# Performance work log

Measured on AMD Instinct MI355X. Metric: run time of the kernel, lower is better.

## Reference

```python
import jax, jax.numpy as jnp
import numpy as np

T, H, W, C, HD, K = 4, 128, 128, 256, 8, 9
F = C // HD


def setup_inputs() -> dict:
    key = jax.random.key(0)
    ks = jax.random.split(key, 6)
    x = jax.random.normal(ks[0], (T, H, W, C), jnp.float32)
    attn = jax.random.uniform(ks[1], (1, HD, T, H, W, K), jnp.float32)
    attn = attn / attn.sum(-1, keepdims=True)  # softmax-normalized neighbor weights
    # integer flow offsets (dt, dh, dw) in [-3, 3], as produced by non-local search
    flows = jax.random.randint(ks[2], (1, HD, T, H, W, K, 3), -3, 4, jnp.int32)
    v_w = jax.random.normal(ks[3], (C, C), jnp.float32) * (C ** -0.5)
    proj_w = jax.random.normal(ks[4], (C, C), jnp.float32) * (C ** -0.5)
    proj_b = jnp.zeros((C,), jnp.float32)
    return dict(x=x, attn=attn, flows=flows, v_w=v_w, proj_w=proj_w, proj_b=proj_b)


def reference(x, attn, flows, v_w, proj_w, proj_b):
    T, H, W, C = x.shape
    HD = attn.shape[1]
    F = C // HD
    # v projection, split heads: [T,H,W,HD,F]
    v = (x @ v_w.T).reshape(T, H, W, HD, F)
    fl = flows[0]  # [HD,T,H,W,K,3] integer offsets (dt, dh, dw)
    tt = jnp.clip(jnp.arange(T)[None, :, None, None, None] + fl[..., 0], 0, T - 1)
    hh = jnp.clip(jnp.arange(H)[None, None, :, None, None] + fl[..., 1], 0, H - 1)
    ww = jnp.clip(jnp.arange(W)[None, None, None, :, None] + fl[..., 2], 0, W - 1)
    hd = jnp.arange(HD)[:, None, None, None, None]
    # flow-guided non-local gather: [HD,T,H,W,K,F]
    gathered = v[tt, hh, ww, hd]
    # attention-weighted sum over K neighbors, merge heads: [T,H,W,C]
    out = jnp.einsum('dthwk,dthwkf->thwdf', attn[0], gathered).reshape(T, H, W, C)
    # output projection
    return out @ proj_w.T + proj_b
```

## Files before the change

### kernel.cpp

```cpp
#include <hip/hip_runtime.h>
#include <hip/hip_bf16.h>

namespace {

constexpr int T = 4, H = 128, W = 128, C = 256, HD = 8, K = 9, F = 32;
constexpr int M = T * H * W;

typedef __attribute__((ext_vector_type(8))) short short8v;
typedef __attribute__((ext_vector_type(4))) float f32x4;

__device__ __forceinline__ unsigned short f2bf(float f) {
  unsigned u = __float_as_uint(f);
  unsigned r = (u + 0x7fffu + ((u >> 16) & 1u)) >> 16;
  return (unsigned short)r;
}

__device__ __forceinline__ float bf2f(unsigned short u) {
  return __uint_as_float(((unsigned)u) << 16);
}

template <int ALAYOUT, bool OUT_F32>
__global__ __launch_bounds__(256) void mfma_gemm(
    const void* __restrict__ Aptr, const float* __restrict__ Bw,
    void* __restrict__ Cptr, const float* __restrict__ bias) {
  __shared__ unsigned short As[128][40];
  __shared__ unsigned short Bs[128][40];
  const int m0 = blockIdx.x * 128;
  const int n0 = blockIdx.y * 128;
  const int t = threadIdx.x;
  const int lane = t & 63;
  const int wid = t >> 6;
  const int wm = wid >> 1, wn = wid & 1;
  const int fr = lane & 15;
  const int kg = lane >> 4;

  f32x4 acc[4][4];
#pragma unroll
  for (int ni = 0; ni < 4; ++ni) {
    float b = 0.f;
    if (OUT_F32) b = bias[n0 + wn * 64 + ni * 16 + fr];
#pragma unroll
    for (int mi = 0; mi < 4; ++mi) {
      acc[mi][ni][0] = b; acc[mi][ni][1] = b;
      acc[mi][ni][2] = b; acc[mi][ni][3] = b;
    }
  }

  for (int k0 = 0; k0 < C; k0 += 32) {
    __syncthreads();
    if (ALAYOUT == 2) {
      const unsigned short* Ab = (const unsigned short*)Aptr;
      const size_t hb = (size_t)(k0 >> 5) * M * 32;
#pragma unroll
      for (int i = 0; i < 2; ++i) {
        const int flat = t + i * 256;
        const int row = flat >> 2, kc = (flat & 3) * 8;
        *(short8v*)&As[row][kc] =
            *(const short8v*)(Ab + hb + (size_t)(m0 + row) * 32 + kc);
      }
    } else {
      const float* Af = (const float*)Aptr;
#pragma unroll
      for (int i = 0; i < 4; ++i) {
        const int flat = t + i * 256;
        const int row = flat >> 3, kc = (flat & 7) * 4;
        const float4 v4 = *(const float4*)(Af + (size_t)(m0 + row) * C + k0 + kc);
        ushort4 o;
        o.x = f2bf(v4.x); o.y = f2bf(v4.y); o.z = f2bf(v4.z); o.w = f2bf(v4.w);
        *(ushort4*)&As[row][kc] = o;
      }
    }
#pragma unroll
    for (int i = 0; i < 4; ++i) {
      const int flat = t + i * 256;
      const int row = flat >> 3, kc = (flat & 7) * 4;
      const float4 v4 = *(const float4*)(Bw + (size_t)(n0 + row) * C + k0 + kc);
      ushort4 o;
      o.x = f2bf(v4.x); o.y = f2bf(v4.y); o.z = f2bf(v4.z); o.w = f2bf(v4.w);
      *(ushort4*)&Bs[row][kc] = o;
    }
    __syncthreads();
    short8v af[4], bfv[4];
#pragma unroll
    for (int mi = 0; mi < 4; ++mi)
      af[mi] = *(const short8v*)&As[wm * 64 + mi * 16 + fr][kg * 8];
#pragma unroll
    for (int ni = 0; ni < 4; ++ni)
      bfv[ni] = *(const short8v*)&Bs[wn * 64 + ni * 16 + fr][kg * 8];
#pragma unroll
    for (int mi = 0; mi < 4; ++mi)
#pragma unroll
      for (int ni = 0; ni < 4; ++ni)
        acc[mi][ni] = __builtin_amdgcn_mfma_f32_16x16x32_bf16(
            af[mi], bfv[ni], acc[mi][ni], 0, 0, 0);
  }

#pragma unroll
  for (int mi = 0; mi < 4; ++mi) {
#pragma unroll
    for (int ni = 0; ni < 4; ++ni) {
      const int gcol = n0 + wn * 64 + ni * 16 + fr;
#pragma unroll
      for (int r = 0; r < 4; ++r) {
        const int grow = m0 + wm * 64 + mi * 16 + kg * 4 + r;
        if (OUT_F32) {
          ((float*)Cptr)[(size_t)grow * C + gcol] = acc[mi][ni][r];
        } else {
          ((unsigned short*)Cptr)[(size_t)grow * C + gcol] = f2bf(acc[mi][ni][r]);
        }
      }
    }
  }
}

struct __attribute__((packed, aligned(4))) I4p { int a, b, c, d; };
struct __attribute__((packed, aligned(4))) I2p { int a, b; };
struct __attribute__((packed, aligned(4))) F4p { float a, b, c, d; };

__global__ __launch_bounds__(256, 4) void gather_lds_kernel(
    const unsigned short* __restrict__ v, const float* __restrict__ attn,
    const int* __restrict__ flows, unsigned short* __restrict__ agg2) {
  __shared__ __align__(16) unsigned short halo[4 * 14 * 14 * 32];
  const int nb = (blockIdx.x & 7) * 256 + (blockIdx.x >> 3);
  const int head = nb & 7;
  const int tile = nb >> 3;
  const int h0 = (tile >> 4) * 8;
  const int w0 = (tile & 15) * 8;
  const int tid = threadIdx.x;
  const int s = tid & 63;
  const int tq = tid >> 6;
  const int h = h0 + (s >> 3);
  const int w = w0 + (s & 7);
  const int m = (tq << 14) | (h << 7) | w;

  const int base = ((head << 16) | m) * K;
  const int fb = base * 3;
  const I4p f0 = *(const I4p*)(flows + fb + 0);
  const I4p f1 = *(const I4p*)(flows + fb + 4);
  const I4p f2 = *(const I4p*)(flows + fb + 8);
  const I4p f3 = *(const I4p*)(flows + fb + 12);
  const I4p f4 = *(const I4p*)(flows + fb + 16);
  const I4p f5 = *(const I4p*)(flows + fb + 20);
  const I2p f6 = *(const I2p*)(flows + fb + 24);
  const int f7 = flows[fb + 26];
  const F4p a0 = *(const F4p*)(attn + base + 0);
  const F4p a1 = *(const F4p*)(attn + base + 4);
  const float a2 = attn[base + 8];

  const unsigned short* vhead = v + head * F;
  auto piece_src = [&](int pi, int& ldsoff) -> const short8v* {
    const int sliver = pi >> 2, j = pi & 3;
    const int tt = sliver / 196;
    const int rem = sliver - tt * 196;
    const int hh = rem / 14;
    const int ww = rem - hh * 14;
    const int hc = min(max(h0 - 3 + hh, 0), H - 1);
    const int wc = min(max(w0 - 3 + ww, 0), W - 1);
    const int sm = (tt << 14) | (hc << 7) | wc;
    const int jj = (j + (sliver >> 1)) & 3;
    ldsoff = sliver * 32 + jj * 8;
    return (const short8v*)(vhead + (size_t)sm * C + j * 8);
  };
  {
    short8v pc[7]; int lo[7];
#pragma unroll
    for (int it = 0; it < 7; ++it) pc[it] = *piece_src(tid + it * 256, lo[it]);
#pragma unroll
    for (int it = 0; it < 7; ++it) *(short8v*)&halo[lo[it]] = pc[it];
  }
  {
    short8v pc[5]; int lo[5];
#pragma unroll
    for (int it = 0; it < 5; ++it)
      pc[it] = *piece_src(1792 + tid + it * 256, lo[it]);
    short8v pt; int lot = 0;
    if (tid < 64) pt = *piece_src(3072 + tid, lot);
#pragma unroll
    for (int it = 0; it < 5; ++it) *(short8v*)&halo[lo[it]] = pc[it];
    if (tid < 64) *(short8v*)&halo[lot] = pt;
  }
  __syncthreads();

  const int d[27] = {f0.a, f0.b, f0.c, f0.d, f1.a, f1.b, f1.c, f1.d,
                     f2.a, f2.b, f2.c, f2.d, f3.a, f3.b, f3.c, f3.d,
                     f4.a, f4.b, f4.c, f4.d, f5.a, f5.b, f5.c, f5.d,
                     f6.a, f6.b, f7};
  const float aw[9] = {a0.a, a0.b, a0.c, a0.d, a1.a, a1.b, a1.c, a1.d, a2};
  int row[9];
#pragma unroll
  for (int k = 0; k < 9; ++k) {
    const int ts = min(max(tq + d[3 * k + 0], 0), T - 1);
    const int hs = min(max(h + d[3 * k + 1], 0), H - 1) - (h0 - 3);
    const int ws = min(max(w + d[3 * k + 2], 0), W - 1) - (w0 - 3);
    row[k] = (ts * 14 + hs) * 14 + ws;
  }

  float acc[32];
#pragma unroll
  for (int i = 0; i < 32; ++i) acc[i] = 0.f;
#pragma unroll
  for (int k = 0; k < 9; ++k) {
    const int rbase = row[k] * 32;
    const int rot = (row[k] >> 1) & 3;
#pragma unroll
    for (int j = 0; j < 4; ++j) {
      const short8v p = *(const short8v*)&halo[rbase + (((j + rot) & 3)) * 8];
#pragma unroll
      for (int e = 0; e < 8; ++e)
        acc[j * 8 + e] += aw[k] * bf2f((unsigned short)p[e]);
    }
  }

  unsigned short* dst = agg2 + ((size_t)head * M + m) * F;
#pragma unroll
  for (int j = 0; j < 4; ++j) {
    short8v o;
#pragma unroll
    for (int e = 0; e < 8; ++e) o[e] = (short)f2bf(acc[j * 8 + e]);
    *(short8v*)(dst + j * 8) = o;
  }
}

__global__ __launch_bounds__(256) void agg_proj_kernel(
    const unsigned short* __restrict__ v, const float* __restrict__ attn,
    const int* __restrict__ flows, const float* __restrict__ proj_w,
    const float* __restrict__ proj_b, float* __restrict__ out) {
  __shared__ float Agg[32][C];
  __shared__ float Bs[32][C];
  const int bid = blockIdx.x;
  const int t = bid >> 9;
  const int h0 = ((bid >> 5) & 15) * 8;
  const int w0 = (bid & 31) * 4;
  const int tid = threadIdx.x;

  const int g = tid >> 3;
  const int f4 = (tid & 7) * 4;
#pragma unroll
  for (int r = 0; r < 8; ++r) {
    const int pi = r * 32 + g;
    const int pos = pi >> 3;
    const int head = pi & 7;
    const int h = h0 + (pos >> 2);
    const int w = w0 + (pos & 3);
    const int base = (((head * T + t) * H + h) * W + w) * K;
    const int fbase = base * 3;
    float4 acc = {0.f, 0.f, 0.f, 0.f};
#pragma unroll
    for (int k = 0; k < K; ++k) {
      const int dt = flows[fbase + k * 3 + 0];
      const int dh = flows[fbase + k * 3 + 1];
      const int dw = flows[fbase + k * 3 + 2];
      const float aw = attn[base + k];
      const int tt = min(max(t + dt, 0), T - 1);
      const int hh = min(max(h + dh, 0), H - 1);
      const int ww = min(max(w + dw, 0), W - 1);
      const int mm = (tt * H + hh) * W + ww;
      const ushort4 r4 = *(const ushort4*)(v + (size_t)mm * C + head * F + f4);
      acc.x += aw * bf2f(r4.x);
      acc.y += aw * bf2f(r4.y);
      acc.z += aw * bf2f(r4.z);
      acc.w += aw * bf2f(r4.w);
    }
    *(float4*)&Agg[pos][head * F + f4] = acc;
  }
  __syncthreads();

  const int tx = tid & 31;
  const int ty = tid >> 5;
  float acc2[4][8];
  {
    const float4 b0 = *(const float4*)(proj_b + tx * 8);
    const float4 b1 = *(const float4*)(proj_b + tx * 8 + 4);
#pragma unroll
    for (int i = 0; i < 4; ++i) {
      acc2[i][0] = b0.x; acc2[i][1] = b0.y; acc2[i][2] = b0.z; acc2[i][3] = b0.w;
      acc2[i][4] = b1.x; acc2[i][5] = b1.y; acc2[i][6] = b1.z; acc2[i][7] = b1.w;
    }
  }
  for (int k0 = 0; k0 < C; k0 += 32) {
#pragma unroll
    for (int i = 0; i < 8; ++i) {
      const float4 w4 = *(const float4*)(proj_w + (size_t)tid * C + k0 + i * 4);
      Bs[i * 4 + 0][tid] = w4.x;
      Bs[i * 4 + 1][tid] = w4.y;
      Bs[i * 4 + 2][tid] = w4.z;
      Bs[i * 4 + 3][tid] = w4.w;
    }
    __syncthreads();
#pragma unroll 4
    for (int kk = 0; kk < 32; ++kk) {
      const float4 bb0 = *(const float4*)&Bs[kk][tx * 8];
      const float4 bb1 = *(const float4*)&Bs[kk][tx * 8 + 4];
      float a[4];
#pragma unroll
      for (int i = 0; i < 4; ++i) a[i] = Agg[ty * 4 + i][k0 + kk];
#pragma unroll
      for (int i = 0; i < 4; ++i) {
        acc2[i][0] += a[i] * bb0.x;
        acc2[i][1] += a[i] * bb0.y;
        acc2[i][2] += a[i] * bb0.z;
        acc2[i][3] += a[i] * bb0.w;
        acc2[i][4] += a[i] * bb1.x;
        acc2[i][5] += a[i] * bb1.y;
        acc2[i][6] += a[i] * bb1.z;
        acc2[i][7] += a[i] * bb1.w;
      }
    }
    __syncthreads();
  }
#pragma unroll
  for (int i = 0; i < 4; ++i) {
    const int pos = ty * 4 + i;
    const int h = h0 + (pos >> 2);
    const int w = w0 + (pos & 3);
    const int m = (t * H + h) * W + w;
    float4 o0, o1;
    o0.x = acc2[i][0]; o0.y = acc2[i][1]; o0.z = acc2[i][2]; o0.w = acc2[i][3];
    o1.x = acc2[i][4]; o1.y = acc2[i][5]; o1.z = acc2[i][6]; o1.w = acc2[i][7];
    *(float4*)(out + (size_t)m * C + tx * 8) = o0;
    *(float4*)(out + (size_t)m * C + tx * 8 + 4) = o1;
  }
}

}

extern "C" void kernel_launch(void* const* d_in, const int* in_sizes, int n_in,
                              void* d_out, int out_size, void* d_ws,
                              size_t ws_size, hipStream_t stream) {
  const float* x = (const float*)d_in[0];
  const float* attn = (const float*)d_in[1];
  const int* flows = (const int*)d_in[2];
  const float* v_w = (const float*)d_in[3];
  const float* proj_w = (const float*)d_in[4];
  const float* proj_b = (const float*)d_in[5];
  float* out = (float*)d_out;

  const size_t VBYTES = (size_t)M * C * 2;
  unsigned short* v = (unsigned short*)d_ws;

  dim3 g1(M / 128, C / 128);
  mfma_gemm<0, false><<<g1, 256, 0, stream>>>(x, v_w, v, nullptr);

  if (ws_size >= 2 * VBYTES) {
    unsigned short* agg2 = (unsigned short*)((char*)d_ws + VBYTES);
    gather_lds_kernel<<<2048, 256, 0, stream>>>(v, attn, flows, agg2);
    mfma_gemm<2, true><<<g1, 256, 0, stream>>>(agg2, proj_w, out, proj_b);
  } else {
    const int nblk = T * (H / 8) * (W / 4);
    agg_proj_kernel<<<nblk, 256, 0, stream>>>(v, attn, flows, proj_w, proj_b,
                                              out);
  }
}
```

Before: 96.92 us.

## Stage flow and attention loads through LDS for coalesced global reads

```diff
diff --git a/kernel.cpp b/kernel.cpp
--- a/kernel.cpp
+++ b/kernel.cpp
@@ -114,13 +114,13 @@
 }
 
 struct __attribute__((packed, aligned(4))) I4p { int a, b, c, d; };
-struct __attribute__((packed, aligned(4))) I2p { int a, b; };
 struct __attribute__((packed, aligned(4))) F4p { float a, b, c, d; };
 
 __global__ __launch_bounds__(256, 4) void gather_lds_kernel(
     const unsigned short* __restrict__ v, const float* __restrict__ attn,
     const int* __restrict__ flows, unsigned short* __restrict__ agg2) {
   __shared__ __align__(16) unsigned short halo[4 * 14 * 14 * 32];
+  int* metaI = (int*)halo;
   const int nb = (blockIdx.x & 7) * 256 + (blockIdx.x >> 3);
   const int head = nb & 7;
   const int tile = nb >> 3;
@@ -132,22 +132,99 @@
   const int h = h0 + (s >> 3);
   const int w = w0 + (s & 7);
   const int m = (tq << 14) | (h << 7) | w;
-
-  const int base = ((head << 16) | m) * K;
-  const int fb = base * 3;
-  const I4p f0 = *(const I4p*)(flows + fb + 0);
-  const I4p f1 = *(const I4p*)(flows + fb + 4);
-  const I4p f2 = *(const I4p*)(flows + fb + 8);
-  const I4p f3 = *(const I4p*)(flows + fb + 12);
-  const I4p f4 = *(const I4p*)(flows + fb + 16);
-  const I4p f5 = *(const I4p*)(flows + fb + 20);
-  const I2p f6 = *(const I2p*)(flows + fb + 24);
-  const int f7 = flows[fb + 26];
-  const F4p a0 = *(const F4p*)(attn + base + 0);
-  const F4p a1 = *(const F4p*)(attn + base + 4);
-  const float a2 = attn[base + 8];
-
   const unsigned short* vhead = v + head * F;
+
+  auto runpair = [&](int r) -> int {
+    return (head << 16) | ((r >> 3) << 14) | ((h0 + (r & 7)) << 7) | w0;
+  };
+
+  I4p fpc[7]; int fr_[7], fq_[7];
+#pragma unroll
+  for (int e = 0; e < 7; ++e) {
+    const int p = tid + e * 256;
+    fr_[e] = -1;
+    if (p < 1728) {
+      const int r = p / 54, q = p - r * 54;
+      fr_[e] = r; fq_[e] = q;
+      fpc[e] = *(const I4p*)(flows + (size_t)runpair(r) * 27 + 4 * q);
+    }
+  }
+  F4p apc[3]; int ar_[3], aq_[3];
+#pragma unroll
+  for (int e = 0; e < 3; ++e) {
+    const int p = tid + e * 256;
+    ar_[e] = -1;
+    if (p < 576) {
+      const int r = p / 18, q = p - r * 18;
+      ar_[e] = r; aq_[e] = q;
+      apc[e] = *(const F4p*)(attn + (size_t)runpair(r) * 9 + 4 * q);
+    }
+  }
+
+#pragma unroll
+  for (int e = 0; e < 7; ++e) {
+    if (fr_[e] >= 0) {
+      const int d0 = 4 * fq_[e];
+      const int j0 = d0 / 27, r1 = d0 - 27 * j0;
+      const int vals[4] = {fpc[e].a, fpc[e].b, fpc[e].c, fpc[e].d};
+#pragma unroll
+      for (int c = 0; c < 4; ++c) {
+        const int rr = r1 + c;
+        const int j = (rr < 27) ? j0 : j0 + 1;
+        const int dd = (rr < 27) ? rr : rr - 27;
+        metaI[fr_[e] * 224 + j * 28 + dd] = vals[c];
+      }
+    }
+  }
+#pragma unroll
+  for (int e = 0; e < 3; ++e) {
+    if (ar_[e] >= 0) {
+      const int d0 = 4 * aq_[e];
+      const int j0 = d0 / 9, r1 = d0 - 9 * j0;
+      const float vals[4] = {apc[e].a, apc[e].b, apc[e].c, apc[e].d};
+#pragma unroll
+      for (int c = 0; c < 4; ++c) {
+        int rr = r1 + c, j = j0;
+        while (rr >= 9) { rr -= 9; ++j; }
+        ((float*)metaI)[7168 + ar_[e] * 96 + j * 12 + rr] = vals[c];
+      }
+    }
+  }
+  __syncthreads();
+
+  const int orun = tid >> 3, oj = tid & 7;
+  int fd[28];
+  {
+    const int base = orun * 224 + oj * 28;
+#pragma unroll
+    for (int e = 0; e < 7; ++e) {
+      const I4p t4 = *(const I4p*)(metaI + base + 4 * e);
+      fd[4 * e + 0] = t4.a; fd[4 * e + 1] = t4.b;
+      fd[4 * e + 2] = t4.c; fd[4 * e + 3] = t4.d;
+    }
+  }
+  float ad[12];
+  {
+    const int base = 7168 + orun * 96 + oj * 12;
+#pragma unroll
+    for (int e = 0; e < 3; ++e) {
+      const F4p t4 = *(const F4p*)((const float*)metaI + base + 4 * e);
+      ad[4 * e + 0] = t4.a; ad[4 * e + 1] = t4.b;
+      ad[4 * e + 2] = t4.c; ad[4 * e + 3] = t4.d;
+    }
+  }
+
+  float aw[9]; int row[9];
+#pragma unroll
+  for (int k = 0; k < 9; ++k) {
+    aw[k] = ad[k];
+    const int ts = min(max(tq + fd[3 * k + 0], 0), T - 1);
+    const int hs = min(max(h + fd[3 * k + 1], 0), H - 1) - (h0 - 3);
+    const int ws = min(max(w + fd[3 * k + 2], 0), W - 1) - (w0 - 3);
+    row[k] = (ts * 14 + hs) * 14 + ws;
+  }
+  __syncthreads();
+
   auto piece_src = [&](int pi, int& ldsoff) -> const short8v* {
     const int sliver = pi >> 2, j = pi & 3;
     const int tt = sliver / 196;
@@ -181,20 +258,6 @@
   }
   __syncthreads();
 
-  const int d[27] = {f0.a, f0.b, f0.c, f0.d, f1.a, f1.b, f1.c, f1.d,
-                     f2.a, f2.b, f2.c, f2.d, f3.a, f3.b, f3.c, f3.d,
-                     f4.a, f4.b, f4.c, f4.d, f5.a, f5.b, f5.c, f5.d,
-                     f6.a, f6.b, f7};
-  const float aw[9] = {a0.a, a0.b, a0.c, a0.d, a1.a, a1.b, a1.c, a1.d, a2};
-  int row[9];
-#pragma unroll
-  for (int k = 0; k < 9; ++k) {
-    const int ts = min(max(tq + d[3 * k + 0], 0), T - 1);
-    const int hs = min(max(h + d[3 * k + 1], 0), H - 1) - (h0 - 3);
-    const int ws = min(max(w + d[3 * k + 2], 0), W - 1) - (w0 - 3);
-    row[k] = (ts * 14 + hs) * 14 + ws;
-  }
-
   float acc[32];
 #pragma unroll
   for (int i = 0; i < 32; ++i) acc[i] = 0.f;
```

After: 102.7 us. 6.0% more time.
